# Kernel optimization log

Measured on AMD Instinct MI355X. Metric: run time of the kernel, lower is better.

Reference implementation:

```python
import jax, jax.numpy as jnp
import numpy as np

FEAT = 256
HID = 512

def _xavier(key, shape):
    fan_in, fan_out = shape
    lim = (6.0 / (fan_in + fan_out)) ** 0.5
    return jax.random.uniform(key, shape, jnp.float32, -lim, lim)

def setup_inputs() -> dict:
    key = jax.random.key(0)
    ks = jax.random.split(key, 9)
    x = jax.random.normal(ks[0], (256, 512, FEAT), jnp.float32)
    W_i = _xavier(ks[1], (FEAT, HID)); U_i = _xavier(ks[2], (HID, HID))
    W_f = _xavier(ks[3], (FEAT, HID)); U_f = _xavier(ks[4], (HID, HID))
    W_c = _xavier(ks[5], (FEAT, HID)); U_c = _xavier(ks[6], (HID, HID))
    W_o = _xavier(ks[7], (FEAT, HID)); U_o = _xavier(ks[8], (HID, HID))
    b = jnp.zeros((HID,), jnp.float32)
    return {"x": x,
            "W_i": W_i, "U_i": U_i, "b_i": b,
            "W_f": W_f, "U_f": U_f, "b_f": b,
            "W_c": W_c, "U_c": U_c, "b_c": b,
            "W_o": W_o, "U_o": U_o, "b_o": b}

def reference(x, W_i, U_i, b_i, W_f, U_f, b_f, W_c, U_c, b_c, W_o, U_o, b_o):
    B, T, _ = x.shape
    H = U_i.shape[0]
    # Batch all input-to-hidden GEMMs across timesteps: [B,T,F] @ [F,4H]
    W = jnp.concatenate([W_i, W_f, W_o, W_c], axis=1)   # [F, 4H]
    U = jnp.concatenate([U_i, U_f, U_o, U_c], axis=1)   # [H, 4H]
    b = jnp.concatenate([b_i, b_f, b_o, b_c])           # [4H]
    xW = jnp.einsum('btf,fg->btg', x, W) + b            # [B, T, 4H]
    xW = jnp.swapaxes(xW, 0, 1)                         # [T, B, 4H]

    def step(carry, xw_t):
        h, c = carry
        g = xw_t + h @ U                                # [B, 4H]
        i_t = jax.nn.sigmoid(g[:, 0*H:1*H])
        f_t = jax.nn.sigmoid(g[:, 1*H:2*H])
        o_t = jax.nn.sigmoid(g[:, 2*H:3*H])
        c_tilde = jnp.tanh(g[:, 3*H:4*H])
        c_new = f_t * c + i_t * c_tilde
        h_new = o_t * jnp.tanh(c_new)
        return (h_new, c_new), h_new

    h0 = jnp.zeros((B, H), x.dtype)
    c0 = jnp.zeros((B, H), x.dtype)
    _, hs = jax.lax.scan(step, (h0, c0), xW)            # hs: [T, B, H]
    return jnp.swapaxes(hs, 0, 1)                       # [B, T, H]
```

## Files before the change

kernel.cpp:

```cpp
#include <hip/hip_runtime.h>
#include <hip/hip_bf16.h>
#include <cstdint>


#define B_   256
#define T_   512
#define F_   256
#define H_   512
#define K_   768
#define NG_  2048
#define AW   776

typedef __attribute__((ext_vector_type(8))) short short8;
typedef __attribute__((ext_vector_type(4))) float f32x4;

#define LOG2E 1.4426950408889634f

static __device__ __forceinline__ unsigned short f2bf(float f) {
  union { float f; unsigned u; } v; v.f = f;
  unsigned r = v.u + 0x7FFFu + ((v.u >> 16) & 1u);
  return (unsigned short)(r >> 16);
}
static __device__ __forceinline__ float sigmoid_f(float x) {
  return __builtin_amdgcn_rcpf(1.f + __expf(-x));
}
static __device__ __forceinline__ float tanh_f(float x) {
  return 1.f - 2.f * __builtin_amdgcn_rcpf(__expf(2.f * x) + 1.f);
}

__global__ void prep_weights(const float* __restrict__ Wi, const float* __restrict__ Wf,
                             const float* __restrict__ Wo, const float* __restrict__ Wc,
                             const float* __restrict__ Ui, const float* __restrict__ Uf,
                             const float* __restrict__ Uo, const float* __restrict__ Uc,
                             unsigned short* __restrict__ BT,
                             unsigned* __restrict__ flags) {
  if (blockIdx.x == 0) {
    unsigned* fp = flags + threadIdx.x * 16;
    unsigned z = 0;
    asm volatile("global_store_dword %0, %1, off sc0 sc1" :: "v"(fp), "v"(z) : "memory");
  }
  int idx = blockIdx.x * 256 + threadIdx.x;
  if (idx >= NG_ * K_) return;
  int col = idx / K_;
  int k   = idx - col * K_;
  int gate = col >> 9;
  int hc   = col & 511;
  const float* Wg = (gate == 0) ? Wi : (gate == 1) ? Wf : (gate == 2) ? Wo : Wc;
  const float* Ug = (gate == 0) ? Ui : (gate == 1) ? Uf : (gate == 2) ? Uo : Uc;
  float v = (k < F_) ? Wg[k * H_ + hc] : Ug[(k - F_) * H_ + hc];
  BT[idx] = f2bf(v);
}

__global__ __launch_bounds__(256, 1)
void lstm_persist(const float* __restrict__ x,
                  const unsigned short* __restrict__ BT,
                  const float* __restrict__ bi, const float* __restrict__ bfp,
                  const float* __restrict__ bo, const float* __restrict__ bc,
                  float* __restrict__ out,
                  unsigned* __restrict__ flags,
                  unsigned short* __restrict__ hbuf) {
  __shared__ __align__(16) unsigned short Ash[32][AW];
  __shared__ float Gsh[4][32][18];

  const int tid = threadIdx.x;
  const int rg = blockIdx.x & 7;
  const int cg = blockIdx.x >> 3;
  const int wave = tid >> 6, lane = tid & 63;
  const int l15 = lane & 15, l4 = lane >> 4;

  short8 Breg[24];
  {
    const unsigned short* Bp =
        BT + (size_t)((wave << 9) | (cg << 4) | l15) * K_ + l4 * 8;
    #pragma unroll
    for (int kk = 0; kk < 24; ++kk)
      Breg[kk] = *reinterpret_cast<const short8*>(Bp + kk * 32);
  }

  const int grow_r = tid >> 3;
  const int gcol0 = (tid & 7) * 2;
  const int hcg = (cg << 4) + gcol0;
  const float bi0 = bi[hcg],  bi1 = bi[hcg + 1];
  const float bf0 = bfp[hcg], bf1 = bfp[hcg + 1];
  const float bo0 = bo[hcg],  bo1 = bo[hcg + 1];
  const float bc0 = bc[hcg],  bc1 = bc[hcg + 1];
  float cc0 = 0.f, cc1 = 0.f;
  const int grow = rg * 32 + grow_r;
  float* outp = out + (size_t)grow * T_ * H_ + hcg;
  unsigned* hbp0 = reinterpret_cast<unsigned*>(hbuf + (size_t)grow * H_ + hcg);
  unsigned* hbp1 = reinterpret_cast<unsigned*>(hbuf + (size_t)(B_ + grow) * H_ + hcg);

  #pragma unroll
  for (int j = 0; j < 8; ++j) {
    int f = tid + 256 * j; int row = f >> 6, k4 = f & 63;
    const float4 v = *reinterpret_cast<const float4*>(
        x + (size_t)(rg * 32 + row) * T_ * F_ + k4 * 4);
    ushort4 s; s.x = f2bf(v.x); s.y = f2bf(v.y); s.z = f2bf(v.z); s.w = f2bf(v.w);
    *reinterpret_cast<ushort4*>(&Ash[row][k4 * 4]) = s;
  }

  unsigned* myflag = flags + (rg * 32 + cg) * 16;
  const unsigned* pollflag = flags + (rg * 32 + (lane >> 1)) * 16;
  const unsigned short* hsrc0 = hbuf;
  const unsigned short* hsrc1 = hbuf + (size_t)B_ * H_;
  const unsigned vo = (unsigned)(((rg * 32 + wave) * H_ + lane * 8) * 2);

  for (int t = 0; t < T_; ++t) {
    if (t > 0) {
      const unsigned want = (unsigned)t;
      unsigned cur;
      do {
        asm volatile("global_load_dword %0, %1, off sc0 sc1\n\ts_waitcnt vmcnt(0)"
                     : "=v"(cur) : "v"(pollflag) : "memory");
      } while (cur < want);
      const unsigned short* hsrc = ((t - 1) & 1) ? hsrc1 : hsrc0;
      short8 h0, h1, h2, h3, h4, h5, h6, h7;
      asm volatile(
        "global_load_dwordx4 %0, %8, %16 sc0 sc1\n\t"
        "global_load_dwordx4 %1, %9, %16 sc0 sc1\n\t"
        "global_load_dwordx4 %2, %10, %16 sc0 sc1\n\t"
        "global_load_dwordx4 %3, %11, %16 sc0 sc1\n\t"
        "global_load_dwordx4 %4, %12, %16 sc0 sc1\n\t"
        "global_load_dwordx4 %5, %13, %16 sc0 sc1\n\t"
        "global_load_dwordx4 %6, %14, %16 sc0 sc1\n\t"
        "global_load_dwordx4 %7, %15, %16 sc0 sc1\n\t"
        "s_waitcnt vmcnt(0)"
        : "=&v"(h0), "=&v"(h1), "=&v"(h2), "=&v"(h3),
          "=&v"(h4), "=&v"(h5), "=&v"(h6), "=&v"(h7)
        : "v"(vo), "v"(vo + 4096u), "v"(vo + 8192u), "v"(vo + 12288u),
          "v"(vo + 16384u), "v"(vo + 20480u), "v"(vo + 24576u), "v"(vo + 28672u),
          "s"(hsrc)
        : "memory");
      *reinterpret_cast<short8*>(&Ash[wave +  0][F_ + lane * 8]) = h0;
      *reinterpret_cast<short8*>(&Ash[wave +  4][F_ + lane * 8]) = h1;
      *reinterpret_cast<short8*>(&Ash[wave +  8][F_ + lane * 8]) = h2;
      *reinterpret_cast<short8*>(&Ash[wave + 12][F_ + lane * 8]) = h3;
      *reinterpret_cast<short8*>(&Ash[wave + 16][F_ + lane * 8]) = h4;
      *reinterpret_cast<short8*>(&Ash[wave + 20][F_ + lane * 8]) = h5;
      *reinterpret_cast<short8*>(&Ash[wave + 24][F_ + lane * 8]) = h6;
      *reinterpret_cast<short8*>(&Ash[wave + 28][F_ + lane * 8]) = h7;
    } else {
      #pragma unroll
      for (int j = 0; j < 8; ++j) {
        int f = tid + 256 * j; int row = f >> 6, c8 = f & 63;
        short8 z = {0, 0, 0, 0, 0, 0, 0, 0};
        *reinterpret_cast<short8*>(&Ash[row][F_ + c8 * 8]) = z;
      }
    }
    __syncthreads();

    float4 xv[8];
    if (t + 1 < T_) {
      #pragma unroll
      for (int j = 0; j < 8; ++j) {
        int f = tid + 256 * j; int row = f >> 6, k4 = f & 63;
        xv[j] = *reinterpret_cast<const float4*>(
            x + ((size_t)(rg * 32 + row) * T_ + (t + 1)) * F_ + k4 * 4);
      }
    }

    f32x4 acc0 = {0, 0, 0, 0}, acc1 = {0, 0, 0, 0};
    #pragma unroll
    for (int kk = 0; kk < 24; ++kk) {
      const int ks = kk * 32 + l4 * 8;
      const short8 a0 = *reinterpret_cast<const short8*>(&Ash[l15][ks]);
      const short8 a1 = *reinterpret_cast<const short8*>(&Ash[16 + l15][ks]);
      acc0 = __builtin_amdgcn_mfma_f32_16x16x32_bf16(a0, Breg[kk], acc0, 0, 0, 0);
      acc1 = __builtin_amdgcn_mfma_f32_16x16x32_bf16(a1, Breg[kk], acc1, 0, 0, 0);
    }
    #pragma unroll
    for (int r = 0; r < 4; ++r) {
      Gsh[wave][l4 * 4 + r][l15]      = acc0[r];
      Gsh[wave][16 + l4 * 4 + r][l15] = acc1[r];
    }
    __syncthreads();

    float h0, h1;
    {
      const float2 Gi = *reinterpret_cast<const float2*>(&Gsh[0][grow_r][gcol0]);
      const float2 Gf = *reinterpret_cast<const float2*>(&Gsh[1][grow_r][gcol0]);
      const float2 Go = *reinterpret_cast<const float2*>(&Gsh[2][grow_r][gcol0]);
      const float2 Gc = *reinterpret_cast<const float2*>(&Gsh[3][grow_r][gcol0]);
      const float it0 = sigmoid_f(Gi.x + bi0), it1 = sigmoid_f(Gi.y + bi1);
      const float ft0 = sigmoid_f(Gf.x + bf0), ft1 = sigmoid_f(Gf.y + bf1);
      const float ot0 = sigmoid_f(Go.x + bo0), ot1 = sigmoid_f(Go.y + bo1);
      const float ct0 = tanh_f(Gc.x + bc0),    ct1 = tanh_f(Gc.y + bc1);
      cc0 = ft0 * cc0 + it0 * ct0;
      cc1 = ft1 * cc1 + it1 * ct1;
      h0 = ot0 * tanh_f(cc0);
      h1 = ot1 * tanh_f(cc1);
      unsigned hp = (unsigned)f2bf(h0) | ((unsigned)f2bf(h1) << 16);
      unsigned* hq = (t & 1) ? hbp1 : hbp0;
      asm volatile("global_store_dword %0, %1, off sc0 sc1"
                   :: "v"(hq), "v"(hp) : "memory");
    }
    asm volatile("s_waitcnt vmcnt(0)" ::: "memory");
    __syncthreads();
    if (tid == 0) {
      unsigned val = (unsigned)(t + 1);
      asm volatile("global_store_dword %0, %1, off sc0 sc1"
                   :: "v"(myflag), "v"(val) : "memory");
    }

    float2 hw; hw.x = h0; hw.y = h1;
    *reinterpret_cast<float2*>(outp + (size_t)t * H_) = hw;
    if (t + 1 < T_) {
      #pragma unroll
      for (int j = 0; j < 8; ++j) {
        int f = tid + 256 * j; int row = f >> 6, k4 = f & 63;
        ushort4 s; s.x = f2bf(xv[j].x); s.y = f2bf(xv[j].y);
        s.z = f2bf(xv[j].z); s.w = f2bf(xv[j].w);
        *reinterpret_cast<ushort4*>(&Ash[row][k4 * 4]) = s;
      }
    }
  }
}

extern "C" void kernel_launch(void* const* d_in, const int* in_sizes, int n_in,
                              void* d_out, int out_size, void* d_ws, size_t ws_size,
                              hipStream_t stream) {
  const float* x  = (const float*)d_in[0];
  const float* Wi = (const float*)d_in[1];
  const float* Ui = (const float*)d_in[2];
  const float* bi = (const float*)d_in[3];
  const float* Wf = (const float*)d_in[4];
  const float* Uf = (const float*)d_in[5];
  const float* bf = (const float*)d_in[6];
  const float* Wc = (const float*)d_in[7];
  const float* Uc = (const float*)d_in[8];
  const float* bc = (const float*)d_in[9];
  const float* Wo = (const float*)d_in[10];
  const float* Uo = (const float*)d_in[11];
  const float* bo = (const float*)d_in[12];
  float* out = (float*)d_out;

  unsigned short* BT = (unsigned short*)d_ws;
  unsigned short* hbuf = (unsigned short*)((char*)d_ws + 0x300000);
  unsigned* flags = (unsigned*)((char*)d_ws + 0x380000);

  prep_weights<<<(NG_ * K_ + 255) / 256, 256, 0, stream>>>(
      Wi, Wf, Wo, Wc, Ui, Uf, Uo, Uc, BT, flags);

  void* args[] = {(void*)&x, (void*)&BT, (void*)&bi, (void*)&bf, (void*)&bo,
                  (void*)&bc, (void*)&out, (void*)&flags, (void*)&hbuf};
  hipLaunchCooperativeKernel(reinterpret_cast<const void*>(&lstm_persist),
                             dim3(256), dim3(256), args, 0, stream);
}
```

Before: 1.483 ms.

## Split GEMM over K across waves and overlap x-part MFMAs with h polling

Each wave now covers all four gates for a K slice instead of one gate over the full K, so the x-input MFMAs can run before waiting on the recurrent h flags. The h slices are loaded from global memory straight into registers as MFMA operands, skipping the LDS staging round-trip. Partial sums are reduced through a larger LDS buffer. The output store is deferred one step, and conversions use hardware packed bf16 instructions. This adds a four-way reduction and an extra barrier per step, and changes the bf16 rounding path.

```diff
diff --git a/kernel.cpp b/kernel.cpp
--- a/kernel.cpp
+++ b/kernel.cpp
@@ -9,12 +9,10 @@
 #define H_   512
 #define K_   768
 #define NG_  2048
-#define AW   776
+#define AWX  264
 
 typedef __attribute__((ext_vector_type(8))) short short8;
 typedef __attribute__((ext_vector_type(4))) float f32x4;
-
-#define LOG2E 1.4426950408889634f
 
 static __device__ __forceinline__ unsigned short f2bf(float f) {
   union { float f; unsigned u; } v; v.f = f;
@@ -27,6 +25,7 @@
 static __device__ __forceinline__ float tanh_f(float x) {
   return 1.f - 2.f * __builtin_amdgcn_rcpf(__expf(2.f * x) + 1.f);
 }
+#define BAR_LDS() asm volatile("s_waitcnt lgkmcnt(0)\n\ts_barrier" ::: "memory")
 
 __global__ void prep_weights(const float* __restrict__ Wi, const float* __restrict__ Wf,
                              const float* __restrict__ Wo, const float* __restrict__ Wc,
@@ -51,6 +50,16 @@
   BT[idx] = f2bf(v);
 }
 
+#define MFMA4(FA, FB, KK)                                                       \
+  g0a = __builtin_amdgcn_mfma_f32_16x16x32_bf16(FA, Brg[0][KK], g0a, 0, 0, 0);  \
+  g0b = __builtin_amdgcn_mfma_f32_16x16x32_bf16(FB, Brg[0][KK], g0b, 0, 0, 0);  \
+  g1a = __builtin_amdgcn_mfma_f32_16x16x32_bf16(FA, Brg[1][KK], g1a, 0, 0, 0);  \
+  g1b = __builtin_amdgcn_mfma_f32_16x16x32_bf16(FB, Brg[1][KK], g1b, 0, 0, 0);  \
+  g2a = __builtin_amdgcn_mfma_f32_16x16x32_bf16(FA, Brg[2][KK], g2a, 0, 0, 0);  \
+  g2b = __builtin_amdgcn_mfma_f32_16x16x32_bf16(FB, Brg[2][KK], g2b, 0, 0, 0);  \
+  g3a = __builtin_amdgcn_mfma_f32_16x16x32_bf16(FA, Brg[3][KK], g3a, 0, 0, 0);  \
+  g3b = __builtin_amdgcn_mfma_f32_16x16x32_bf16(FB, Brg[3][KK], g3b, 0, 0, 0)
+
 __global__ __launch_bounds__(256, 1)
 void lstm_persist(const float* __restrict__ x,
                   const unsigned short* __restrict__ BT,
@@ -59,22 +68,25 @@
                   float* __restrict__ out,
                   unsigned* __restrict__ flags,
                   unsigned short* __restrict__ hbuf) {
-  __shared__ __align__(16) unsigned short Ash[32][AW];
-  __shared__ float Gsh[4][32][18];
+  __shared__ __align__(16) unsigned short Ash[32][AWX];
+  __shared__ float Gsh[4][4][32][18];
 
   const int tid = threadIdx.x;
   const int rg = blockIdx.x & 7;
   const int cg = blockIdx.x >> 3;
   const int wave = tid >> 6, lane = tid & 63;
+  const int wk = wave;
   const int l15 = lane & 15, l4 = lane >> 4;
 
-  short8 Breg[24];
-  {
-    const unsigned short* Bp =
-        BT + (size_t)((wave << 9) | (cg << 4) | l15) * K_ + l4 * 8;
+  short8 Brg[4][6];
+  #pragma unroll
+  for (int g = 0; g < 4; ++g) {
+    const unsigned short* Bp = BT + (size_t)((g << 9) | (cg << 4) | l15) * K_;
     #pragma unroll
-    for (int kk = 0; kk < 24; ++kk)
-      Breg[kk] = *reinterpret_cast<const short8*>(Bp + kk * 32);
+    for (int kk = 0; kk < 6; ++kk) {
+      const int k = (kk < 2) ? (wk * 64 + kk * 32) : (256 + wk * 128 + (kk - 2) * 32);
+      Brg[g][kk] = *reinterpret_cast<const short8*>(Bp + k + l4 * 8);
+    }
   }
 
   const int grow_r = tid >> 3;
@@ -85,135 +97,145 @@
   const float bo0 = bo[hcg],  bo1 = bo[hcg + 1];
   const float bc0 = bc[hcg],  bc1 = bc[hcg + 1];
   float cc0 = 0.f, cc1 = 0.f;
+  float h0v = 0.f, h1v = 0.f;
   const int grow = rg * 32 + grow_r;
   float* outp = out + (size_t)grow * T_ * H_ + hcg;
   unsigned* hbp0 = reinterpret_cast<unsigned*>(hbuf + (size_t)grow * H_ + hcg);
   unsigned* hbp1 = reinterpret_cast<unsigned*>(hbuf + (size_t)(B_ + grow) * H_ + hcg);
+
+  const unsigned voA = (unsigned)(((rg * 32 + l15) * H_ + wk * 128 + l4 * 8) * 2);
+  const unsigned voB = voA + (unsigned)(16 * H_ * 2);
+  const unsigned short* hsrc0 = hbuf;
+  const unsigned short* hsrc1 = hbuf + (size_t)B_ * H_;
+  unsigned* myflag = flags + (rg * 32 + cg) * 16;
+  const unsigned* pollp = flags + (rg * 32 + wk * 8 + (lane & 7)) * 16;
 
   #pragma unroll
   for (int j = 0; j < 8; ++j) {
     int f = tid + 256 * j; int row = f >> 6, k4 = f & 63;
     const float4 v = *reinterpret_cast<const float4*>(
         x + (size_t)(rg * 32 + row) * T_ * F_ + k4 * 4);
-    ushort4 s; s.x = f2bf(v.x); s.y = f2bf(v.y); s.z = f2bf(v.z); s.w = f2bf(v.w);
-    *reinterpret_cast<ushort4*>(&Ash[row][k4 * 4]) = s;
-  }
-
-  unsigned* myflag = flags + (rg * 32 + cg) * 16;
-  const unsigned* pollflag = flags + (rg * 32 + (lane >> 1)) * 16;
-  const unsigned short* hsrc0 = hbuf;
-  const unsigned short* hsrc1 = hbuf + (size_t)B_ * H_;
-  const unsigned vo = (unsigned)(((rg * 32 + wave) * H_ + lane * 8) * 2);
+    unsigned lo, hi;
+    asm("v_cvt_pk_bf16_f32 %0, %1, %2" : "=v"(lo) : "v"(v.x), "v"(v.y));
+    asm("v_cvt_pk_bf16_f32 %0, %1, %2" : "=v"(hi) : "v"(v.z), "v"(v.w));
+    uint2 p; p.x = lo; p.y = hi;
+    *reinterpret_cast<uint2*>(&Ash[row][k4 * 4]) = p;
+  }
+  __syncthreads();
 
   for (int t = 0; t < T_; ++t) {
+    f32x4 g0a = {0,0,0,0}, g0b = {0,0,0,0}, g1a = {0,0,0,0}, g1b = {0,0,0,0};
+    f32x4 g2a = {0,0,0,0}, g2b = {0,0,0,0}, g3a = {0,0,0,0}, g3b = {0,0,0,0};
+
+    {
+      const short8 xa0 = *reinterpret_cast<const short8*>(&Ash[l15][wk * 64 + l4 * 8]);
+      const short8 xb0 = *reinterpret_cast<const short8*>(&Ash[16 + l15][wk * 64 + l4 * 8]);
+      MFMA4(xa0, xb0, 0);
+      const short8 xa1 = *reinterpret_cast<const short8*>(&Ash[l15][wk * 64 + 32 + l4 * 8]);
+      const short8 xb1 = *reinterpret_cast<const short8*>(&Ash[16 + l15][wk * 64 + 32 + l4 * 8]);
+      MFMA4(xa1, xb1, 1);
+    }
+
+    float4 xv[8];
+    if (t + 1 < T_) {
+      #pragma unroll
+      for (int j = 0; j < 8; ++j) {
+        xv[j] = *reinterpret_cast<const float4*>(
+            x + ((size_t)(rg * 32 + wave + 4 * j) * T_ + (t + 1)) * F_ + lane * 4);
+      }
+    }
+
+    short8 hA0, hA1, hA2, hA3, hB0, hB1, hB2, hB3;
     if (t > 0) {
       const unsigned want = (unsigned)t;
       unsigned cur;
       do {
         asm volatile("global_load_dword %0, %1, off sc0 sc1\n\ts_waitcnt vmcnt(0)"
-                     : "=v"(cur) : "v"(pollflag) : "memory");
+                     : "=v"(cur) : "v"(pollp) : "memory");
       } while (cur < want);
       const unsigned short* hsrc = ((t - 1) & 1) ? hsrc1 : hsrc0;
-      short8 h0, h1, h2, h3, h4, h5, h6, h7;
       asm volatile(
-        "global_load_dwordx4 %0, %8, %16 sc0 sc1\n\t"
-        "global_load_dwordx4 %1, %9, %16 sc0 sc1\n\t"
-        "global_load_dwordx4 %2, %10, %16 sc0 sc1\n\t"
-        "global_load_dwordx4 %3, %11, %16 sc0 sc1\n\t"
-        "global_load_dwordx4 %4, %12, %16 sc0 sc1\n\t"
-        "global_load_dwordx4 %5, %13, %16 sc0 sc1\n\t"
-        "global_load_dwordx4 %6, %14, %16 sc0 sc1\n\t"
-        "global_load_dwordx4 %7, %15, %16 sc0 sc1\n\t"
+        "global_load_dwordx4 %0, %8, %10 sc0 sc1\n\t"
+        "global_load_dwordx4 %1, %8, %10 offset:64 sc0 sc1\n\t"
+        "global_load_dwordx4 %2, %8, %10 offset:128 sc0 sc1\n\t"
+        "global_load_dwordx4 %3, %8, %10 offset:192 sc0 sc1\n\t"
+        "global_load_dwordx4 %4, %9, %10 sc0 sc1\n\t"
+        "global_load_dwordx4 %5, %9, %10 offset:64 sc0 sc1\n\t"
+        "global_load_dwordx4 %6, %9, %10 offset:128 sc0 sc1\n\t"
+        "global_load_dwordx4 %7, %9, %10 offset:192 sc0 sc1\n\t"
         "s_waitcnt vmcnt(0)"
-        : "=&v"(h0), "=&v"(h1), "=&v"(h2), "=&v"(h3),
-          "=&v"(h4), "=&v"(h5), "=&v"(h6), "=&v"(h7)
-        : "v"(vo), "v"(vo + 4096u), "v"(vo + 8192u), "v"(vo + 12288u),
-          "v"(vo + 16384u), "v"(vo + 20480u), "v"(vo + 24576u), "v"(vo + 28672u),
-          "s"(hsrc)
+        : "=&v"(hA0), "=&v"(hA1), "=&v"(hA2), "=&v"(hA3),
+          "=&v"(hB0), "=&v"(hB1), "=&v"(hB2), "=&v"(hB3)
+        : "v"(voA), "v"(voB), "s"(hsrc)
         : "memory");
-      *reinterpret_cast<short8*>(&Ash[wave +  0][F_ + lane * 8]) = h0;
-      *reinterpret_cast<short8*>(&Ash[wave +  4][F_ + lane * 8]) = h1;
-      *reinterpret_cast<short8*>(&Ash[wave +  8][F_ + lane * 8]) = h2;
-      *reinterpret_cast<short8*>(&Ash[wave + 12][F_ + lane * 8]) = h3;
-      *reinterpret_cast<short8*>(&Ash[wave + 16][F_ + lane * 8]) = h4;
-      *reinterpret_cast<short8*>(&Ash[wave + 20][F_ + lane * 8]) = h5;
-      *reinterpret_cast<short8*>(&Ash[wave + 24][F_ + lane * 8]) = h6;
-      *reinterpret_cast<short8*>(&Ash[wave + 28][F_ + lane * 8]) = h7;
-    } else {
-      #pragma unroll
-      for (int j = 0; j < 8; ++j) {
-        int f = tid + 256 * j; int row = f >> 6, c8 = f & 63;
-        short8 z = {0, 0, 0, 0, 0, 0, 0, 0};
-        *reinterpret_cast<short8*>(&Ash[row][F_ + c8 * 8]) = z;
-      }
-    }
-    __syncthreads();
-
-    float4 xv[8];
-    if (t + 1 < T_) {
-      #pragma unroll
-      for (int j = 0; j < 8; ++j) {
-        int f = tid + 256 * j; int row = f >> 6, k4 = f & 63;
-        xv[j] = *reinterpret_cast<const float4*>(
-            x + ((size_t)(rg * 32 + row) * T_ + (t + 1)) * F_ + k4 * 4);
-      }
-    }
-
-    f32x4 acc0 = {0, 0, 0, 0}, acc1 = {0, 0, 0, 0};
-    #pragma unroll
-    for (int kk = 0; kk < 24; ++kk) {
-      const int ks = kk * 32 + l4 * 8;
-      const short8 a0 = *reinterpret_cast<const short8*>(&Ash[l15][ks]);
-      const short8 a1 = *reinterpret_cast<const short8*>(&Ash[16 + l15][ks]);
-      acc0 = __builtin_amdgcn_mfma_f32_16x16x32_bf16(a0, Breg[kk], acc0, 0, 0, 0);
-      acc1 = __builtin_amdgcn_mfma_f32_16x16x32_bf16(a1, Breg[kk], acc1, 0, 0, 0);
-    }
+      __builtin_amdgcn_sched_barrier(0);
+
+      MFMA4(hA0, hB0, 2);
+      MFMA4(hA1, hB1, 3);
+      MFMA4(hA2, hB2, 4);
+      MFMA4(hA3, hB3, 5);
+      float2 hw; hw.x = h0v; hw.y = h1v;
+      *reinterpret_cast<float2*>(outp + (size_t)(t - 1) * H_) = hw;
+    }
+
     #pragma unroll
     for (int r = 0; r < 4; ++r) {
-      Gsh[wave][l4 * 4 + r][l15]      = acc0[r];
-      Gsh[wave][16 + l4 * 4 + r][l15] = acc1[r];
-    }
-    __syncthreads();
-
-    float h0, h1;
+      Gsh[wk][0][l4 * 4 + r][l15] = g0a[r]; Gsh[wk][0][16 + l4 * 4 + r][l15] = g0b[r];
+      Gsh[wk][1][l4 * 4 + r][l15] = g1a[r]; Gsh[wk][1][16 + l4 * 4 + r][l15] = g1b[r];
+      Gsh[wk][2][l4 * 4 + r][l15] = g2a[r]; Gsh[wk][2][16 + l4 * 4 + r][l15] = g2b[r];
+      Gsh[wk][3][l4 * 4 + r][l15] = g3a[r]; Gsh[wk][3][16 + l4 * 4 + r][l15] = g3b[r];
+    }
+    BAR_LDS();
+
     {
-      const float2 Gi = *reinterpret_cast<const float2*>(&Gsh[0][grow_r][gcol0]);
-      const float2 Gf = *reinterpret_cast<const float2*>(&Gsh[1][grow_r][gcol0]);
-      const float2 Go = *reinterpret_cast<const float2*>(&Gsh[2][grow_r][gcol0]);
-      const float2 Gc = *reinterpret_cast<const float2*>(&Gsh[3][grow_r][gcol0]);
-      const float it0 = sigmoid_f(Gi.x + bi0), it1 = sigmoid_f(Gi.y + bi1);
-      const float ft0 = sigmoid_f(Gf.x + bf0), ft1 = sigmoid_f(Gf.y + bf1);
-      const float ot0 = sigmoid_f(Go.x + bo0), ot1 = sigmoid_f(Go.y + bo1);
-      const float ct0 = tanh_f(Gc.x + bc0),    ct1 = tanh_f(Gc.y + bc1);
+      float gi0 = bi0, gi1 = bi1, gf0 = bf0, gf1 = bf1;
+      float go0 = bo0, go1 = bo1, gc0 = bc0, gc1 = bc1;
+      #pragma unroll
+      for (int w = 0; w < 4; ++w) {
+        const float2 a = *reinterpret_cast<const float2*>(&Gsh[w][0][grow_r][gcol0]);
+        const float2 b = *reinterpret_cast<const float2*>(&Gsh[w][1][grow_r][gcol0]);
+        const float2 c = *reinterpret_cast<const float2*>(&Gsh[w][2][grow_r][gcol0]);
+        const float2 d = *reinterpret_cast<const float2*>(&Gsh[w][3][grow_r][gcol0]);
+        gi0 += a.x; gi1 += a.y; gf0 += b.x; gf1 += b.y;
+        go0 += c.x; go1 += c.y; gc0 += d.x; gc1 += d.y;
+      }
+      const float it0 = sigmoid_f(gi0), it1 = sigmoid_f(gi1);
+      const float ft0 = sigmoid_f(gf0), ft1 = sigmoid_f(gf1);
+      const float ot0 = sigmoid_f(go0), ot1 = sigmoid_f(go1);
+      const float ct0 = tanh_f(gc0),    ct1 = tanh_f(gc1);
       cc0 = ft0 * cc0 + it0 * ct0;
       cc1 = ft1 * cc1 + it1 * ct1;
-      h0 = ot0 * tanh_f(cc0);
-      h1 = ot1 * tanh_f(cc1);
-      unsigned hp = (unsigned)f2bf(h0) | ((unsigned)f2bf(h1) << 16);
+      h0v = ot0 * tanh_f(cc0);
+      h1v = ot1 * tanh_f(cc1);
+      unsigned hp;
+      asm("v_cvt_pk_bf16_f32 %0, %1, %2" : "=v"(hp) : "v"(h0v), "v"(h1v));
       unsigned* hq = (t & 1) ? hbp1 : hbp0;
       asm volatile("global_store_dword %0, %1, off sc0 sc1"
                    :: "v"(hq), "v"(hp) : "memory");
     }
     asm volatile("s_waitcnt vmcnt(0)" ::: "memory");
-    __syncthreads();
+    BAR_LDS();
     if (tid == 0) {
       unsigned val = (unsigned)(t + 1);
       asm volatile("global_store_dword %0, %1, off sc0 sc1"
                    :: "v"(myflag), "v"(val) : "memory");
     }
 
-    float2 hw; hw.x = h0; hw.y = h1;
-    *reinterpret_cast<float2*>(outp + (size_t)t * H_) = hw;
     if (t + 1 < T_) {
       #pragma unroll
       for (int j = 0; j < 8; ++j) {
-        int f = tid + 256 * j; int row = f >> 6, k4 = f & 63;
-        ushort4 s; s.x = f2bf(xv[j].x); s.y = f2bf(xv[j].y);
-        s.z = f2bf(xv[j].z); s.w = f2bf(xv[j].w);
-        *reinterpret_cast<ushort4*>(&Ash[row][k4 * 4]) = s;
+        unsigned lo, hi;
+        asm("v_cvt_pk_bf16_f32 %0, %1, %2" : "=v"(lo) : "v"(xv[j].x), "v"(xv[j].y));
+        asm("v_cvt_pk_bf16_f32 %0, %1, %2" : "=v"(hi) : "v"(xv[j].z), "v"(xv[j].w));
+        uint2 p; p.x = lo; p.y = hi;
+        *reinterpret_cast<uint2*>(&Ash[wave + 4 * j][lane * 4]) = p;
       }
     }
-  }
+    BAR_LDS();
+  }
+
+  float2 hw; hw.x = h0v; hw.y = h1v;
+  *reinterpret_cast<float2*>(outp + (size_t)(T_ - 1) * H_) = hw;
 }
 
 extern "C" void kernel_launch(void* const* d_in, const int* in_sizes, int n_in,
```

New measurement: 1.987 ms. 34.0% more time.
